# Kernel tuning notes

Hardware: AMD Instinct MI355X
Metric: run time of the kernel (lower is better)

## Reference

```python
import jax, jax.numpy as jnp
import numpy as np
from functools import partial

N_NODES = 50000
N_EDGES = 600000
N_FEAT = 128
HID = [128, 64, 32, 16]
N_GRAPHS = 64
N_CLASSES = 10


def gcn_conv(x, W, b, src, dst, n_nodes):
    # PyG GCNConv: h = x @ W; propagate with symmetric norm over A + I; add bias.
    h = x @ W  # [N, out]
    ones = jnp.ones((src.shape[0],), dtype=x.dtype)
    deg = jax.ops.segment_sum(ones, dst, num_segments=n_nodes) + 1.0  # self-loop
    dinv = jax.lax.rsqrt(deg)
    coef = dinv[src] * dinv[dst]  # [E]
    agg = jax.ops.segment_sum(h[src] * coef[:, None], dst, num_segments=n_nodes)
    agg = agg + h * (dinv * dinv)[:, None]  # self-loop contribution
    return agg + b


def global_mean_pool(x, batch, n_graphs):
    s = jax.ops.segment_sum(x, batch, num_segments=n_graphs)
    cnt = jax.ops.segment_sum(jnp.ones((x.shape[0],), x.dtype), batch, num_segments=n_graphs)
    return s / jnp.maximum(cnt, 1.0)[:, None]


def setup_inputs() -> dict:
    key = jax.random.key(0)
    ks = jax.random.split(key, 16)
    x = jax.random.normal(ks[0], (N_NODES, N_FEAT), dtype=jnp.float32)
    edge_index = jax.random.randint(ks[1], (2, N_EDGES), 0, N_NODES, dtype=jnp.int64)
    batch = jnp.sort(jax.random.randint(ks[2], (N_NODES,), 0, N_GRAPHS, dtype=jnp.int64))

    def glorot(k, fan_in, fan_out):
        s = float(np.sqrt(6.0 / (fan_in + fan_out)))
        return jax.random.uniform(k, (fan_in, fan_out), jnp.float32, -s, s)

    dims = [N_FEAT] + HID
    params = {}
    for i in range(4):
        params[f"W{i+1}"] = glorot(ks[3 + i], dims[i], dims[i + 1])
        params[f"b{i+1}"] = jnp.zeros((dims[i + 1],), jnp.float32)
    params["Wlin"] = glorot(ks[7], HID[-1], N_CLASSES)
    params["blin"] = jnp.zeros((N_CLASSES,), jnp.float32)
    return {"x": x, "edge_index": edge_index, "batch": batch, **params}


def reference(x, edge_index, batch, W1, b1, W2, b2, W3, b3, W4, b4, Wlin, blin):
    src, dst = edge_index[0], edge_index[1]
    n = x.shape[0]
    h = jax.nn.relu(gcn_conv(x, W1, b1, src, dst, n))
    h = jax.nn.relu(gcn_conv(h, W2, b2, src, dst, n))
    h = jax.nn.relu(gcn_conv(h, W3, b3, src, dst, n))
    h = jax.nn.relu(gcn_conv(h, W4, b4, src, dst, n))
    g = global_mean_pool(h, batch, N_GRAPHS)  # [G, 16]
    return g @ Wlin + blin
```

## Files before the change

### kernel.cpp

```cpp
#include <hip/hip_runtime.h>
#include <hip/hip_bf16.h>


#define N_GRAPHS 64
#define N_CLASSES 10

typedef short bf8_t __attribute__((ext_vector_type(8)));
typedef float f4_t  __attribute__((ext_vector_type(4)));

__device__ __forceinline__ float b2f(unsigned int u) {
  return __uint_as_float(u << 16);
}
__device__ __forceinline__ unsigned short f2b(float f) {
  unsigned int x = __float_as_uint(f);
  x += 0x7fffu + ((x >> 16) & 1u);
  return (unsigned short)(x >> 16);
}

__device__ __forceinline__ void block_detect(const unsigned int* __restrict__ xraw,
    const unsigned int* __restrict__ eraw, int* f32, int* i64) {
  __shared__ int c_bf, c_nz;
  if (threadIdx.x == 0) { c_bf = 0; c_nz = 0; }
  __syncthreads();
  unsigned int d = xraw[threadIdx.x & 255];
  int e = (int)(((d & 0xffffu) >> 7) & 0xff);
  if (e >= 100 && e <= 140) atomicAdd(&c_bf, 1);
  if (eraw && threadIdx.x < 64 && eraw[2 * threadIdx.x + 1] != 0u) atomicAdd(&c_nz, 1);
  __syncthreads();
  *f32 = (c_bf < 150) ? 1 : 0;
  if (i64) *i64 = (c_nz == 0) ? 1 : 0;
}

struct WPtrs { const void* p[10]; };
static constexpr int WSEG[10] = {16384, 128, 8192, 64, 2048, 32, 512, 16, 160, 10};
static constexpr int WTOTAL   = 27546;
static constexpr int WOFF[10] = {0, 16384, 16512, 24704, 24768, 26816, 26848, 27360, 27376, 27536};

__global__ __launch_bounds__(256) void cvtwe_kernel(
    const unsigned int* __restrict__ xraw, WPtrs wp, unsigned short* __restrict__ wc,
    const int* __restrict__ braw, int* __restrict__ b32,
    const int* __restrict__ eraw, int* __restrict__ deg, int* __restrict__ rank,
    unsigned short* __restrict__ xb,
    int BE2, int XC, int BW, int n, int E) {
  int f32, i64;
  block_detect(xraw, (const unsigned int*)eraw, &f32, &i64);
  const int bid = blockIdx.x;
  if (bid < BE2) {
    #pragma unroll
    for (int r = 0; r < 2; ++r) {
      int e = bid * 512 + r * 256 + threadIdx.x;
      if (e < E) {
        int d = i64 ? eraw[2 * (E + e)] : eraw[E + e];
        rank[e] = atomicAdd(&deg[d], 1);
      }
    }
  } else if (bid < BE2 + XC) {
    int i = (bid - BE2) * 2048 + threadIdx.x * 8;
    if (i < n * 128) {
      if (f32) {
        float4 u0 = *(const float4*)((const float*)xraw + i);
        float4 u1 = *(const float4*)((const float*)xraw + i + 4);
        uint4 o;
        o.x = (unsigned int)f2b(u0.x) | ((unsigned int)f2b(u0.y) << 16);
        o.y = (unsigned int)f2b(u0.z) | ((unsigned int)f2b(u0.w) << 16);
        o.z = (unsigned int)f2b(u1.x) | ((unsigned int)f2b(u1.y) << 16);
        o.w = (unsigned int)f2b(u1.z) | ((unsigned int)f2b(u1.w) << 16);
        *(uint4*)&xb[i] = o;
      } else {
        *(uint4*)&xb[i] = *(const uint4*)((const unsigned short*)xraw + i);
      }
    }
  } else if (bid < BE2 + XC + BW) {
    int i = (bid - BE2 - XC) * 256 + threadIdx.x;
    if (i >= WTOTAL) return;
    int off = i, s = 0;
    #pragma unroll
    for (int t = 0; t < 10; ++t) {
      if (s == 0 && off >= WSEG[t]) { off -= WSEG[t]; } else if (s == 0) { s = t + 1; }
    }
    s -= 1;
    int soff = off;
    if ((s & 1) == 0 && s <= 6) {
      int KB, FOUT;
      if (s == 0)      { KB = 4; FOUT = 128; }
      else if (s == 2) { KB = 4; FOUT = 64; }
      else if (s == 4) { KB = 2; FOUT = 32; }
      else             { KB = 1; FOUT = 16; }
      int j = off & 7, l = (off >> 3) & 63, f = off >> 9;
      int ct = f / KB, kb = f - ct * KB;
      int k = kb * 32 + ((l >> 4) << 3) + j;
      int nn = ct * 16 + (l & 15);
      soff = k * FOUT + nn;
    }
    const void* p = wp.p[s];
    wc[WOFF[s] + off] = f32 ? f2b(((const float*)p)[soff])
                            : ((const unsigned short*)p)[soff];
  } else {
    int i = (bid - BE2 - XC - BW) * 256 + threadIdx.x;
    if (i < n) b32[i] = i64 ? braw[2 * i] : braw[i];
  }
}

__global__ __launch_bounds__(256) void scan_kernel(const int* __restrict__ deg,
    int* __restrict__ row_ptr, float* __restrict__ dinv,
    unsigned long long* __restrict__ desc, uint2* __restrict__ csr, int n) {
  __shared__ int ws[4];
  __shared__ int s_total;
  __shared__ unsigned int s_prev;
  const int b = blockIdx.x, tid = threadIdx.x, lane = tid & 63, wv = tid >> 6;
  const int i = b * 256 + tid;
  int v = (i < n) ? (deg[i] + 1) : 0;
  int x = v;
  #pragma unroll
  for (int off = 1; off < 64; off <<= 1) {
    int y = __shfl_up(x, off, 64);
    if (lane >= off) x += y;
  }
  if (lane == 63) ws[wv] = x;
  __syncthreads();
  int wbase = 0;
  for (int w = 0; w < wv; ++w) wbase += ws[w];
  int incl = x + wbase;
  if (tid == 0) {
    int tot = ws[0] + ws[1] + ws[2] + ws[3];
    s_total = tot;
    unsigned long long st = (b == 0) ? (2ULL << 62) : (1ULL << 62);
    atomicExch(&desc[b], st | (unsigned long long)(unsigned int)tot);
    if (b == 0) s_prev = 0u;
  }
  __syncthreads();
  if (b > 0 && wv == 0) {
    unsigned int running = 0;
    int j = b - 1;
    while (true) {
      int idx = j - lane;
      unsigned long long d;
      if (idx >= 0) {
        do { d = atomicAdd(&desc[idx], 0ULL); } while ((d >> 62) == 0ULL);
      } else {
        d = (2ULL << 62);
      }
      unsigned long long ball = __ballot((d >> 62) == 2ULL);
      int fp = ball ? (__ffsll((unsigned long long)ball) - 1) : 64;
      unsigned int contrib = (lane <= fp) ? (unsigned int)(d & 0xffffffffULL) : 0u;
      #pragma unroll
      for (int o = 32; o; o >>= 1) contrib += __shfl_xor(contrib, o, 64);
      running += contrib;
      if (fp < 64) break;
      j -= 64;
    }
    if (lane == 0) {
      atomicExch(&desc[b], (2ULL << 62) |
                 (unsigned long long)(unsigned int)(running + (unsigned int)s_total));
      s_prev = running;
    }
  }
  __syncthreads();
  int tot = (int)s_prev + incl;
  if (i < n) {
    row_ptr[i + 1] = tot;
    float di = rsqrtf((float)v);
    dinv[i] = di;
    uint2 se;
    se.x = (unsigned int)i;
    se.y = __float_as_uint(di * di);
    csr[tot - v] = se;
  }
  if (i == 0) row_ptr[0] = 0;
}

__global__ __launch_bounds__(256) void fill_kernel(
    const int* __restrict__ eraw, const unsigned int* __restrict__ xraw,
    const int* __restrict__ row_ptr, const int* __restrict__ rank,
    const float* __restrict__ dinv, uint2* __restrict__ csr, int E) {
  int f32, i64;
  block_detect(xraw, (const unsigned int*)eraw, &f32, &i64);
  int e = blockIdx.x * 256 + threadIdx.x;
  if (e >= E) return;
  int s, d;
  if (i64) { s = eraw[2 * e]; d = eraw[2 * (E + e)]; }
  else     { s = eraw[e];     d = eraw[E + e]; }
  int pos = row_ptr[d] + 1 + rank[e];
  uint2 v;
  v.x = (unsigned int)s;
  v.y = __float_as_uint(dinv[s] * dinv[d]);
  csr[pos] = v;
}

template<int DW> struct UVec { unsigned int d[DW]; };
template<int DW>
__device__ __forceinline__ UVec<DW> uload(const unsigned int* p) {
  UVec<DW> r;
  if constexpr (DW == 4) { uint4 v = *(const uint4*)p; r.d[0]=v.x; r.d[1]=v.y; r.d[2]=v.z; r.d[3]=v.w; }
  else if constexpr (DW == 2) { uint2 v = *(const uint2*)p; r.d[0]=v.x; r.d[1]=v.y; }
  else { r.d[0] = *p; }
  return r;
}
template<int DW>
__device__ __forceinline__ void ustore(unsigned int* p, const UVec<DW>& v) {
  if constexpr (DW == 4) { *(uint4*)p = make_uint4(v.d[0], v.d[1], v.d[2], v.d[3]); }
  else if constexpr (DW == 2) { *(uint2*)p = make_uint2(v.d[0], v.d[1]); }
  else { *p = v.d[0]; }
}

__global__ __launch_bounds__(256) void aggemm0_kernel(
    const unsigned short* __restrict__ Xb,
    const int* __restrict__ row_ptr, const uint2* __restrict__ csr,
    const unsigned short* __restrict__ wc,
    unsigned short* __restrict__ Hout, int n) {
  constexpr int LPG = 16, DW = 4, LD = 136;
  __shared__ unsigned short T[16 * LD];
  __shared__ unsigned short T2[16 * LD];
  const int r = threadIdx.x / LPG, l = threadIdx.x % LPG;
  const int node0 = blockIdx.x * 16;
  const int g = node0 + r;
  const unsigned int* H2 = (const unsigned int*)Xb;
  UVec<DW> o;
  #pragma unroll
  for (int d = 0; d < DW; ++d) o.d[d] = 0u;
  if (g < n) {
    float a[2 * DW];
    #pragma unroll
    for (int d = 0; d < 2 * DW; ++d) a[d] = 0.f;
    const int e0 = row_ptr[g], e1 = row_ptr[g + 1];
    for (int base = e0; base < e1; base += LPG) {
      int cnt = e1 - base < LPG ? e1 - base : LPG;
      uint2 my = csr[(base + l < e1) ? (base + l) : (e1 - 1)];
      for (int j0 = 0; j0 < cnt; j0 += 4) {
        int   sj[4];
        float cj[4];
        #pragma unroll
        for (int jj = 0; jj < 4; ++jj) {
          int j = j0 + jj;
          sj[jj] = __shfl((int)my.x, j & (LPG - 1), LPG);
          float cc = __uint_as_float(__shfl((int)my.y, j & (LPG - 1), LPG));
          cj[jj] = (j < cnt) ? cc : 0.f;
        }
        UVec<DW> v[4];
        #pragma unroll
        for (int jj = 0; jj < 4; ++jj)
          v[jj] = uload<DW>(H2 + (size_t)sj[jj] * 64 + l * DW);
        #pragma unroll
        for (int jj = 0; jj < 4; ++jj) {
          #pragma unroll
          for (int d = 0; d < DW; ++d) {
            a[2*d]   = fmaf(b2f(v[jj].d[d] & 0xffffu), cj[jj], a[2*d]);
            a[2*d+1] = fmaf(b2f(v[jj].d[d] >> 16),     cj[jj], a[2*d+1]);
          }
        }
      }
    }
    #pragma unroll
    for (int d = 0; d < DW; ++d)
      o.d[d] = (unsigned int)f2b(a[2*d]) | ((unsigned int)f2b(a[2*d+1]) << 16);
  }
  ustore<DW>((unsigned int*)&T[r * LD + l * DW * 2], o);
  __syncthreads();
  const int w = threadIdx.x >> 6;
  const int ll = threadIdx.x & 63;
  const int l15 = ll & 15, quad = ll >> 4;
  const unsigned short* W1f = wc + WOFF[0];
  const unsigned short* b1  = wc + WOFF[1];
  const unsigned short* W2f = wc + WOFF[2];
  #pragma unroll
  for (int c = 0; c < 2; ++c) {
    const int ct1 = w * 2 + c;
    f4_t acc = {0.f, 0.f, 0.f, 0.f};
    #pragma unroll
    for (int kb = 0; kb < 4; ++kb) {
      bf8_t afr = *(const bf8_t*)&T[l15 * LD + kb * 32 + quad * 8];
      bf8_t bfr = *(const bf8_t*)&W1f[((ct1 * 4 + kb) * 64 + ll) * 8];
      acc = __builtin_amdgcn_mfma_f32_16x16x32_bf16(afr, bfr, acc, 0, 0, 0);
    }
    float bv = b2f(b1[ct1 * 16 + l15]);
    #pragma unroll
    for (int rr = 0; rr < 4; ++rr)
      T2[(quad * 4 + rr) * LD + ct1 * 16 + l15] = f2b(fmaxf(acc[rr] + bv, 0.f));
  }
  __syncthreads();
  f4_t a2 = {0.f, 0.f, 0.f, 0.f};
  #pragma unroll
  for (int kb = 0; kb < 4; ++kb) {
    bf8_t afr = *(const bf8_t*)&T2[l15 * LD + kb * 32 + quad * 8];
    bf8_t bfr = *(const bf8_t*)&W2f[((w * 4 + kb) * 64 + ll) * 8];
    a2 = __builtin_amdgcn_mfma_f32_16x16x32_bf16(afr, bfr, a2, 0, 0, 0);
  }
  #pragma unroll
  for (int rr = 0; rr < 4; ++rr) {
    int node = node0 + quad * 4 + rr;
    if (node < n)
      Hout[(size_t)node * 64 + w * 16 + l15] = f2b(a2[rr]);
  }
}

template<int FIN, int FOUT, int LPG>
__global__ __launch_bounds__(256) void aggemm_kernel(
    const unsigned short* __restrict__ Hin,
    const int* __restrict__ row_ptr, const uint2* __restrict__ csr,
    const unsigned short* __restrict__ bias,
    const unsigned short* __restrict__ Wf, unsigned short* __restrict__ Hout, int n) {
  constexpr int DW  = FIN / LPG / 2;
  constexpr int NPB = 256 / LPG;
  constexpr int LD  = FIN + 8;
  constexpr int KB  = FIN / 32;
  constexpr int CT  = FOUT / 16;
  constexpr int MT  = NPB / 16;
  __shared__ unsigned short T[NPB * LD];
  const int r = threadIdx.x / LPG, l = threadIdx.x % LPG;
  const int node0 = blockIdx.x * NPB;
  const int g = node0 + r;
  const unsigned int* H2 = (const unsigned int*)Hin;
  UVec<DW> o;
  #pragma unroll
  for (int d = 0; d < DW; ++d) o.d[d] = 0u;
  if (g < n) {
    float a[2 * DW];
    #pragma unroll
    for (int d = 0; d < 2 * DW; ++d) a[d] = 0.f;
    const int e0 = row_ptr[g], e1 = row_ptr[g + 1];
    for (int base = e0; base < e1; base += LPG) {
      int cnt = e1 - base < LPG ? e1 - base : LPG;
      uint2 my = csr[(base + l < e1) ? (base + l) : (e1 - 1)];
      for (int j0 = 0; j0 < cnt; j0 += 4) {
        int   sj[4];
        float cj[4];
        #pragma unroll
        for (int jj = 0; jj < 4; ++jj) {
          int j = j0 + jj;
          sj[jj] = __shfl((int)my.x, j & (LPG - 1), LPG);
          float cc = __uint_as_float(__shfl((int)my.y, j & (LPG - 1), LPG));
          cj[jj] = (j < cnt) ? cc : 0.f;
        }
        UVec<DW> v[4];
        #pragma unroll
        for (int jj = 0; jj < 4; ++jj)
          v[jj] = uload<DW>(H2 + (size_t)sj[jj] * (FIN / 2) + l * DW);
        #pragma unroll
        for (int jj = 0; jj < 4; ++jj) {
          #pragma unroll
          for (int d = 0; d < DW; ++d) {
            a[2*d]   = fmaf(b2f(v[jj].d[d] & 0xffffu), cj[jj], a[2*d]);
            a[2*d+1] = fmaf(b2f(v[jj].d[d] >> 16),     cj[jj], a[2*d+1]);
          }
        }
      }
    }
    UVec<DW> bb = uload<DW>((const unsigned int*)bias + l * DW);
    #pragma unroll
    for (int d = 0; d < DW; ++d) {
      float lo = fmaxf(a[2*d]   + b2f(bb.d[d] & 0xffffu), 0.f);
      float hi = fmaxf(a[2*d+1] + b2f(bb.d[d] >> 16), 0.f);
      o.d[d] = (unsigned int)f2b(lo) | ((unsigned int)f2b(hi) << 16);
    }
  }
  ustore<DW>((unsigned int*)&T[r * LD + l * DW * 2], o);
  __syncthreads();
  const int w = threadIdx.x >> 6;
  if (w < MT * CT && node0 < n) {
    const int mt = w / CT, ct = w % CT;
    const int ll = threadIdx.x & 63;
    const int r16 = ll & 15, quad = ll >> 4;
    bf8_t afrag[KB], bfrag[KB];
    #pragma unroll
    for (int kb = 0; kb < KB; ++kb) {
      afrag[kb] = *(const bf8_t*)(&T[(mt * 16 + r16) * LD + quad * 8 + kb * 32]);
      bfrag[kb] = *(const bf8_t*)(Wf + ((ct * KB + kb) * 64 + ll) * 8);
    }
    f4_t acc = {0.f, 0.f, 0.f, 0.f};
    #pragma unroll
    for (int kb = 0; kb < KB; ++kb)
      acc = __builtin_amdgcn_mfma_f32_16x16x32_bf16(afrag[kb], bfrag[kb], acc, 0, 0, 0);
    #pragma unroll
    for (int rr = 0; rr < 4; ++rr) {
      int node = node0 + mt * 16 + quad * 4 + rr;
      if (node < n)
        Hout[(size_t)node * FOUT + ct * 16 + r16] = f2b(acc[rr]);
    }
  }
}

__global__ __launch_bounds__(256) void agg_pool_kernel(
    const unsigned short* __restrict__ Hin,
    const int* __restrict__ row_ptr, const uint2* __restrict__ csr,
    const unsigned short* __restrict__ bias,
    const int* __restrict__ batch, float* __restrict__ pooled,
    float* __restrict__ cnt, int n) {
  __shared__ float acc[N_GRAPHS * 16];
  __shared__ float ccnt[N_GRAPHS];
  for (int i = threadIdx.x; i < N_GRAPHS * 16; i += 256) acc[i] = 0.f;
  if (threadIdx.x < N_GRAPHS) ccnt[threadIdx.x] = 0.f;
  __syncthreads();
  const int r = threadIdx.x >> 3, l = threadIdx.x & 7;
  const int g = blockIdx.x * 32 + r;
  if (g < n) {
    const unsigned int* H2 = (const unsigned int*)Hin;
    float a0 = 0.f, a1 = 0.f;
    const int e0 = row_ptr[g], e1 = row_ptr[g + 1];
    for (int base = e0; base < e1; base += 8) {
      uint2 eb[8];
      #pragma unroll
      for (int j = 0; j < 8; ++j)
        eb[j] = csr[(base + j < e1) ? (base + j) : (e1 - 1)];
      float cj[8];
      unsigned int v[8];
      #pragma unroll
      for (int j = 0; j < 8; ++j)
        cj[j] = (base + j < e1) ? __uint_as_float(eb[j].y) : 0.f;
      #pragma unroll
      for (int j = 0; j < 8; ++j)
        v[j] = H2[(size_t)eb[j].x * 8 + l];
      #pragma unroll
      for (int j = 0; j < 8; ++j) {
        a0 = fmaf(b2f(v[j] & 0xffffu), cj[j], a0);
        a1 = fmaf(b2f(v[j] >> 16),     cj[j], a1);
      }
    }
    unsigned int bb = ((const unsigned int*)bias)[l];
    a0 = fmaxf(a0 + b2f(bb & 0xffffu), 0.f);
    a1 = fmaxf(a1 + b2f(bb >> 16), 0.f);
    int gb = batch[g];
    atomicAdd(&acc[gb * 16 + l * 2 + 0], a0);
    atomicAdd(&acc[gb * 16 + l * 2 + 1], a1);
    if (l == 0) atomicAdd(&ccnt[gb], 1.f);
  }
  __syncthreads();
  for (int i = threadIdx.x; i < N_GRAPHS * 16; i += 256)
    if (acc[i] != 0.f) atomicAdd(&pooled[i], acc[i]);
  if (threadIdx.x < N_GRAPHS && ccnt[threadIdx.x] != 0.f)
    atomicAdd(&cnt[threadIdx.x], ccnt[threadIdx.x]);
}

__global__ __launch_bounds__(256) void final_kernel(const float* __restrict__ pooled,
    const float* __restrict__ cnt, const unsigned short* __restrict__ wc,
    void* __restrict__ out, const unsigned int* __restrict__ xraw) {
  int f32;
  block_detect(xraw, nullptr, &f32, nullptr);
  int id = blockIdx.x * 256 + threadIdx.x;
  if (id >= N_GRAPHS * N_CLASSES) return;
  const unsigned short* Wlin = wc + WOFF[8];
  const unsigned short* blin = wc + WOFF[9];
  int g = id / N_CLASSES, c = id - g * N_CLASSES;
  float inv = 1.0f / fmaxf(cnt[g], 1.0f);
  float a = b2f(blin[c]);
  #pragma unroll
  for (int f = 0; f < 16; ++f)
    a = fmaf(pooled[g * 16 + f] * inv, b2f(Wlin[f * N_CLASSES + c]), a);
  if (f32) ((float*)out)[id] = a;
  else     ((unsigned short*)out)[id] = f2b(a);
}

extern "C" void kernel_launch(void* const* d_in, const int* in_sizes, int n_in,
                              void* d_out, int out_size, void* d_ws, size_t ws_size,
                              hipStream_t stream) {
  const unsigned int* xraw = (const unsigned int*)d_in[0];
  const int* eraw          = (const int*)d_in[1];
  const int* braw          = (const int*)d_in[2];

  const int N = in_sizes[2];
  const int E = in_sizes[1] / 2;
  const int nb = (N + 255) / 256;

  char* p = (char*)d_ws;
  auto alloc = [&](size_t bytes) -> void* {
    void* r = (void*)p;
    p += (bytes + 255) & ~(size_t)255;
    return r;
  };
  const size_t off_desc = ((size_t)N * 4 + 255) & ~(size_t)255;
  const size_t off_pool = (off_desc + (size_t)nb * 8 + 255) & ~(size_t)255;
  const size_t ztotal   = off_pool + (N_GRAPHS * 16 + N_GRAPHS) * 4;
  char* zbase = (char*)alloc(ztotal);
  int*   deg    = (int*)zbase;
  unsigned long long* desc = (unsigned long long*)(zbase + off_desc);
  float* pooled = (float*)(zbase + off_pool);
  float* cntf   = pooled + N_GRAPHS * 16;

  int*   row_ptr  = (int*)  alloc((size_t)(N + 1) * 4);
  int*   rank     = (int*)  alloc((size_t)E * 4);
  float* dinv     = (float*)alloc((size_t)N * 4);
  int*   batch32  = (int*)  alloc((size_t)N * 4);
  uint2* csr      = (uint2*)alloc((size_t)(E + N + 8) * 8);
  unsigned short* wcan  = (unsigned short*)alloc((size_t)WTOTAL * 2);
  unsigned short* xb    = (unsigned short*)alloc((size_t)N * 128 * 2);
  unsigned short* hbufA = (unsigned short*)alloc((size_t)N * 128 * 2);
  unsigned short* hbufB = (unsigned short*)alloc((size_t)N * 128 * 2);

  hipMemsetAsync(zbase, 0, ztotal, stream);

  WPtrs wp;
  for (int i = 0; i < 10; ++i) wp.p[i] = d_in[3 + i];

  const int BW  = (WTOTAL + 255) / 256;
  const int BB  = nb;
  const int BE  = (E + 255) / 256;
  const int BE2 = (E + 511) / 512;
  const int XC  = (N * 128 + 2047) / 2048;
  cvtwe_kernel<<<BE2 + XC + BW + BB, 256, 0, stream>>>(xraw, wp, wcan,
      braw, batch32, eraw, deg, rank, xb, BE2, XC, BW, N, E);

  scan_kernel<<<nb, 256, 0, stream>>>(deg, row_ptr, dinv, desc, csr, N);

  const unsigned short* b2 = wcan + WOFF[3];
  const unsigned short* W3 = wcan + WOFF[4];
  const unsigned short* b3 = wcan + WOFF[5];
  const unsigned short* W4 = wcan + WOFF[6];
  const unsigned short* b4 = wcan + WOFF[7];

  fill_kernel<<<BE, 256, 0, stream>>>(eraw, xraw, row_ptr, rank, dinv, csr, E);

  aggemm0_kernel<<<(N + 15) / 16, 256, 0, stream>>>(
      xb, row_ptr, csr, wcan, hbufB, N);
  aggemm_kernel<64, 32, 8><<<(N + 31) / 32, 256, 0, stream>>>(
      hbufB, row_ptr, csr, b2, W3, hbufA, N);
  aggemm_kernel<32, 16, 8><<<(N + 31) / 32, 256, 0, stream>>>(
      hbufA, row_ptr, csr, b3, W4, hbufB, N);
  agg_pool_kernel<<<(N + 31) / 32, 256, 0, stream>>>(hbufB, row_ptr, csr, b4,
      batch32, pooled, cntf, N);

  final_kernel<<<(N_GRAPHS * N_CLASSES + 255) / 256, 256, 0, stream>>>(pooled, cntf, wcan, d_out, xraw);
}
```

Baseline: 208.0 us.

## Split edge atomics into own kernel and fuse scan with conversion work

```diff
diff --git a/kernel.cpp b/kernel.cpp
--- a/kernel.cpp
+++ b/kernel.cpp
@@ -36,26 +36,98 @@
 static constexpr int WTOTAL   = 27546;
 static constexpr int WOFF[10] = {0, 16384, 16512, 24704, 24768, 26816, 26848, 27360, 27376, 27536};
 
-__global__ __launch_bounds__(256) void cvtwe_kernel(
-    const unsigned int* __restrict__ xraw, WPtrs wp, unsigned short* __restrict__ wc,
+__global__ __launch_bounds__(256) void edge_atomic_kernel(
+    const unsigned int* __restrict__ xraw, const int* __restrict__ eraw,
+    int* __restrict__ deg, int* __restrict__ rank, int E) {
+  int f32, i64;
+  block_detect(xraw, (const unsigned int*)eraw, &f32, &i64);
+  #pragma unroll
+  for (int r = 0; r < 4; ++r) {
+    int e = blockIdx.x * 1024 + r * 256 + threadIdx.x;
+    if (e < E) {
+      int d = i64 ? eraw[2 * (E + e)] : eraw[E + e];
+      rank[e] = atomicAdd(&deg[d], 1);
+    }
+  }
+}
+
+__global__ __launch_bounds__(256) void scan_cvt_kernel(const int* __restrict__ deg,
+    int* __restrict__ row_ptr, float* __restrict__ dinv,
+    unsigned long long* __restrict__ desc, uint2* __restrict__ csr,
+    const unsigned int* __restrict__ xraw, const int* __restrict__ eraw,
+    WPtrs wp, unsigned short* __restrict__ wc,
     const int* __restrict__ braw, int* __restrict__ b32,
-    const int* __restrict__ eraw, int* __restrict__ deg, int* __restrict__ rank,
     unsigned short* __restrict__ xb,
-    int BE2, int XC, int BW, int n, int E) {
+    int nb, int XC, int BW, int n) {
   int f32, i64;
   block_detect(xraw, (const unsigned int*)eraw, &f32, &i64);
   const int bid = blockIdx.x;
-  if (bid < BE2) {
-    #pragma unroll
-    for (int r = 0; r < 2; ++r) {
-      int e = bid * 512 + r * 256 + threadIdx.x;
-      if (e < E) {
-        int d = i64 ? eraw[2 * (E + e)] : eraw[E + e];
-        rank[e] = atomicAdd(&deg[d], 1);
+  if (bid < nb) {
+    __shared__ int ws[4];
+    __shared__ int s_total;
+    __shared__ unsigned int s_prev;
+    const int b = bid, tid = threadIdx.x, lane = tid & 63, wv = tid >> 6;
+    const int i = b * 256 + tid;
+    int v = (i < n) ? (deg[i] + 1) : 0;
+    int x = v;
+    #pragma unroll
+    for (int off = 1; off < 64; off <<= 1) {
+      int y = __shfl_up(x, off, 64);
+      if (lane >= off) x += y;
+    }
+    if (lane == 63) ws[wv] = x;
+    __syncthreads();
+    int wbase = 0;
+    for (int w = 0; w < wv; ++w) wbase += ws[w];
+    int incl = x + wbase;
+    if (tid == 0) {
+      int tot = ws[0] + ws[1] + ws[2] + ws[3];
+      s_total = tot;
+      unsigned long long st = (b == 0) ? (2ULL << 62) : (1ULL << 62);
+      atomicExch(&desc[b], st | (unsigned long long)(unsigned int)tot);
+      if (b == 0) s_prev = 0u;
+    }
+    __syncthreads();
+    if (b > 0 && wv == 0) {
+      unsigned int running = 0;
+      int j = b - 1;
+      while (true) {
+        int idx = j - lane;
+        unsigned long long d;
+        if (idx >= 0) {
+          do { d = atomicAdd(&desc[idx], 0ULL); } while ((d >> 62) == 0ULL);
+        } else {
+          d = (2ULL << 62);
+        }
+        unsigned long long ball = __ballot((d >> 62) == 2ULL);
+        int fp = ball ? (__ffsll((unsigned long long)ball) - 1) : 64;
+        unsigned int contrib = (lane <= fp) ? (unsigned int)(d & 0xffffffffULL) : 0u;
+        #pragma unroll
+        for (int o = 32; o; o >>= 1) contrib += __shfl_xor(contrib, o, 64);
+        running += contrib;
+        if (fp < 64) break;
+        j -= 64;
       }
-    }
-  } else if (bid < BE2 + XC) {
-    int i = (bid - BE2) * 2048 + threadIdx.x * 8;
+      if (lane == 0) {
+        atomicExch(&desc[b], (2ULL << 62) |
+                   (unsigned long long)(unsigned int)(running + (unsigned int)s_total));
+        s_prev = running;
+      }
+    }
+    __syncthreads();
+    int tot = (int)s_prev + incl;
+    if (i < n) {
+      row_ptr[i + 1] = tot;
+      float di = rsqrtf((float)v);
+      dinv[i] = di;
+      uint2 se;
+      se.x = (unsigned int)i;
+      se.y = __float_as_uint(di * di);
+      csr[tot - v] = se;
+    }
+    if (i == 0) row_ptr[0] = 0;
+  } else if (bid < nb + XC) {
+    int i = (bid - nb) * 2048 + threadIdx.x * 8;
     if (i < n * 128) {
       if (f32) {
         float4 u0 = *(const float4*)((const float*)xraw + i);
@@ -70,8 +142,8 @@
         *(uint4*)&xb[i] = *(const uint4*)((const unsigned short*)xraw + i);
       }
     }
-  } else if (bid < BE2 + XC + BW) {
-    int i = (bid - BE2 - XC) * 256 + threadIdx.x;
+  } else if (bid < nb + XC + BW) {
+    int i = (bid - nb - XC) * 256 + threadIdx.x;
     if (i >= WTOTAL) return;
     int off = i, s = 0;
     #pragma unroll
@@ -96,77 +168,9 @@
     wc[WOFF[s] + off] = f32 ? f2b(((const float*)p)[soff])
                             : ((const unsigned short*)p)[soff];
   } else {
-    int i = (bid - BE2 - XC - BW) * 256 + threadIdx.x;
+    int i = (bid - nb - XC - BW) * 256 + threadIdx.x;
     if (i < n) b32[i] = i64 ? braw[2 * i] : braw[i];
   }
-}
-
-__global__ __launch_bounds__(256) void scan_kernel(const int* __restrict__ deg,
-    int* __restrict__ row_ptr, float* __restrict__ dinv,
-    unsigned long long* __restrict__ desc, uint2* __restrict__ csr, int n) {
-  __shared__ int ws[4];
-  __shared__ int s_total;
-  __shared__ unsigned int s_prev;
-  const int b = blockIdx.x, tid = threadIdx.x, lane = tid & 63, wv = tid >> 6;
-  const int i = b * 256 + tid;
-  int v = (i < n) ? (deg[i] + 1) : 0;
-  int x = v;
-  #pragma unroll
-  for (int off = 1; off < 64; off <<= 1) {
-    int y = __shfl_up(x, off, 64);
-    if (lane >= off) x += y;
-  }
-  if (lane == 63) ws[wv] = x;
-  __syncthreads();
-  int wbase = 0;
-  for (int w = 0; w < wv; ++w) wbase += ws[w];
-  int incl = x + wbase;
-  if (tid == 0) {
-    int tot = ws[0] + ws[1] + ws[2] + ws[3];
-    s_total = tot;
-    unsigned long long st = (b == 0) ? (2ULL << 62) : (1ULL << 62);
-    atomicExch(&desc[b], st | (unsigned long long)(unsigned int)tot);
-    if (b == 0) s_prev = 0u;
-  }
-  __syncthreads();
-  if (b > 0 && wv == 0) {
-    unsigned int running = 0;
-    int j = b - 1;
-    while (true) {
-      int idx = j - lane;
-      unsigned long long d;
-      if (idx >= 0) {
-        do { d = atomicAdd(&desc[idx], 0ULL); } while ((d >> 62) == 0ULL);
-      } else {
-        d = (2ULL << 62);
-      }
-      unsigned long long ball = __ballot((d >> 62) == 2ULL);
-      int fp = ball ? (__ffsll((unsigned long long)ball) - 1) : 64;
-      unsigned int contrib = (lane <= fp) ? (unsigned int)(d & 0xffffffffULL) : 0u;
-      #pragma unroll
-      for (int o = 32; o; o >>= 1) contrib += __shfl_xor(contrib, o, 64);
-      running += contrib;
-      if (fp < 64) break;
-      j -= 64;
-    }
-    if (lane == 0) {
-      atomicExch(&desc[b], (2ULL << 62) |
-                 (unsigned long long)(unsigned int)(running + (unsigned int)s_total));
-      s_prev = running;
-    }
-  }
-  __syncthreads();
-  int tot = (int)s_prev + incl;
-  if (i < n) {
-    row_ptr[i + 1] = tot;
-    float di = rsqrtf((float)v);
-    dinv[i] = di;
-    uint2 se;
-    se.x = (unsigned int)i;
-    se.y = __float_as_uint(di * di);
-    csr[tot - v] = se;
-  }
-  if (i == 0) row_ptr[0] = 0;
 }
 
 __global__ __launch_bounds__(256) void fill_kernel(
@@ -203,6 +207,39 @@
   else { *p = v.d[0]; }
 }
 
+template<int DW, int LPG>
+__device__ __forceinline__ void gather_shfl(
+    const unsigned int* __restrict__ H2, int FPD,
+    const uint2* __restrict__ csr, int e0, int e1, int l, float* a) {
+  for (int base = e0; base < e1; base += LPG) {
+    int cnt = e1 - base < LPG ? e1 - base : LPG;
+    uint2 my = csr[(base + l < e1) ? (base + l) : (e1 - 1)];
+    for (int j0 = 0; j0 < cnt; j0 += 4) {
+      int   sj[4];
+      float cj[4];
+      #pragma unroll
+      for (int jj = 0; jj < 4; ++jj) {
+        int j = j0 + jj;
+        sj[jj] = __shfl((int)my.x, j & (LPG - 1), LPG);
+        float cc = __uint_as_float(__shfl((int)my.y, j & (LPG - 1), LPG));
+        cj[jj] = (j < cnt) ? cc : 0.f;
+      }
+      UVec<DW> v[4];
+      #pragma unroll
+      for (int jj = 0; jj < 4; ++jj)
+        v[jj] = uload<DW>(H2 + (size_t)sj[jj] * FPD + l * DW);
+      #pragma unroll
+      for (int jj = 0; jj < 4; ++jj) {
+        #pragma unroll
+        for (int d = 0; d < DW; ++d) {
+          a[2*d]   = fmaf(b2f(v[jj].d[d] & 0xffffu), cj[jj], a[2*d]);
+          a[2*d+1] = fmaf(b2f(v[jj].d[d] >> 16),     cj[jj], a[2*d+1]);
+        }
+      }
+    }
+  }
+}
+
 __global__ __launch_bounds__(256) void aggemm0_kernel(
     const unsigned short* __restrict__ Xb,
     const int* __restrict__ row_ptr, const uint2* __restrict__ csr,
@@ -214,7 +251,6 @@
   const int r = threadIdx.x / LPG, l = threadIdx.x % LPG;
   const int node0 = blockIdx.x * 16;
   const int g = node0 + r;
-  const unsigned int* H2 = (const unsigned int*)Xb;
   UVec<DW> o;
   #pragma unroll
   for (int d = 0; d < DW; ++d) o.d[d] = 0u;
@@ -222,34 +258,8 @@
     float a[2 * DW];
     #pragma unroll
     for (int d = 0; d < 2 * DW; ++d) a[d] = 0.f;
-    const int e0 = row_ptr[g], e1 = row_ptr[g + 1];
-    for (int base = e0; base < e1; base += LPG) {
-      int cnt = e1 - base < LPG ? e1 - base : LPG;
-      uint2 my = csr[(base + l < e1) ? (base + l) : (e1 - 1)];
-      for (int j0 = 0; j0 < cnt; j0 += 4) {
-        int   sj[4];
-        float cj[4];
-        #pragma unroll
-        for (int jj = 0; jj < 4; ++jj) {
-          int j = j0 + jj;
-          sj[jj] = __shfl((int)my.x, j & (LPG - 1), LPG);
-          float cc = __uint_as_float(__shfl((int)my.y, j & (LPG - 1), LPG));
-          cj[jj] = (j < cnt) ? cc : 0.f;
-        }
-        UVec<DW> v[4];
-        #pragma unroll
-        for (int jj = 0; jj < 4; ++jj)
-          v[jj] = uload<DW>(H2 + (size_t)sj[jj] * 64 + l * DW);
-        #pragma unroll
-        for (int jj = 0; jj < 4; ++jj) {
-          #pragma unroll
-          for (int d = 0; d < DW; ++d) {
-            a[2*d]   = fmaf(b2f(v[jj].d[d] & 0xffffu), cj[jj], a[2*d]);
-            a[2*d+1] = fmaf(b2f(v[jj].d[d] >> 16),     cj[jj], a[2*d+1]);
-          }
-        }
-      }
-    }
+    gather_shfl<DW, LPG>((const unsigned int*)Xb, 64, csr,
+                         row_ptr[g], row_ptr[g + 1], l, a);
     #pragma unroll
     for (int d = 0; d < DW; ++d)
       o.d[d] = (unsigned int)f2b(a[2*d]) | ((unsigned int)f2b(a[2*d+1]) << 16);
@@ -309,7 +319,6 @@
   const int r = threadIdx.x / LPG, l = threadIdx.x % LPG;
   const int node0 = blockIdx.x * NPB;
   const int g = node0 + r;
-  const unsigned int* H2 = (const unsigned int*)Hin;
   UVec<DW> o;
   #pragma unroll
   for (int d = 0; d < DW; ++d) o.d[d] = 0u;
@@ -317,34 +326,8 @@
     float a[2 * DW];
     #pragma unroll
     for (int d = 0; d < 2 * DW; ++d) a[d] = 0.f;
-    const int e0 = row_ptr[g], e1 = row_ptr[g + 1];
-    for (int base = e0; base < e1; base += LPG) {
-      int cnt = e1 - base < LPG ? e1 - base : LPG;
-      uint2 my = csr[(base + l < e1) ? (base + l) : (e1 - 1)];
-      for (int j0 = 0; j0 < cnt; j0 += 4) {
-        int   sj[4];
-        float cj[4];
-        #pragma unroll
-        for (int jj = 0; jj < 4; ++jj) {
-          int j = j0 + jj;
-          sj[jj] = __shfl((int)my.x, j & (LPG - 1), LPG);
-          float cc = __uint_as_float(__shfl((int)my.y, j & (LPG - 1), LPG));
-          cj[jj] = (j < cnt) ? cc : 0.f;
-        }
-        UVec<DW> v[4];
-        #pragma unroll
-        for (int jj = 0; jj < 4; ++jj)
-          v[jj] = uload<DW>(H2 + (size_t)sj[jj] * (FIN / 2) + l * DW);
-        #pragma unroll
-        for (int jj = 0; jj < 4; ++jj) {
-          #pragma unroll
-          for (int d = 0; d < DW; ++d) {
-            a[2*d]   = fmaf(b2f(v[jj].d[d] & 0xffffu), cj[jj], a[2*d]);
-            a[2*d+1] = fmaf(b2f(v[jj].d[d] >> 16),     cj[jj], a[2*d+1]);
-          }
-        }
-      }
-    }
+    gather_shfl<DW, LPG>((const unsigned int*)Hin, FIN / 2, csr,
+                         row_ptr[g], row_ptr[g + 1], l, a);
     UVec<DW> bb = uload<DW>((const unsigned int*)bias + l * DW);
     #pragma unroll
     for (int d = 0; d < DW; ++d) {
@@ -479,7 +462,7 @@
   int*   rank     = (int*)  alloc((size_t)E * 4);
   float* dinv     = (float*)alloc((size_t)N * 4);
   int*   batch32  = (int*)  alloc((size_t)N * 4);
-  uint2* csr      = (uint2*)alloc((size_t)(E + N + 8) * 8);
+  uint2* csr      = (uint2*)alloc((size_t)(E + N + 16) * 8);
   unsigned short* wcan  = (unsigned short*)alloc((size_t)WTOTAL * 2);
   unsigned short* xb    = (unsigned short*)alloc((size_t)N * 128 * 2);
   unsigned short* hbufA = (unsigned short*)alloc((size_t)N * 128 * 2);
@@ -493,12 +476,13 @@
   const int BW  = (WTOTAL + 255) / 256;
   const int BB  = nb;
   const int BE  = (E + 255) / 256;
-  const int BE2 = (E + 511) / 512;
+  const int BE4 = (E + 1023) / 1024;
   const int XC  = (N * 128 + 2047) / 2048;
-  cvtwe_kernel<<<BE2 + XC + BW + BB, 256, 0, stream>>>(xraw, wp, wcan,
-      braw, batch32, eraw, deg, rank, xb, BE2, XC, BW, N, E);
-
-  scan_kernel<<<nb, 256, 0, stream>>>(deg, row_ptr, dinv, desc, csr, N);
+
+  edge_atomic_kernel<<<BE4, 256, 0, stream>>>(xraw, eraw, deg, rank, E);
+
+  scan_cvt_kernel<<<nb + XC + BW + BB, 256, 0, stream>>>(deg, row_ptr, dinv,
+      desc, csr, xraw, eraw, wp, wcan, braw, batch32, xb, nb, XC, BW, N);
 
   const unsigned short* b2 = wcan + WOFF[3];
   const unsigned short* W3 = wcan + WOFF[4];
```

Measured after the change: 212.8 us. 2.3% more time.
